# Performance work log

Measured on AMD Instinct MI355X. Metric: run time of the kernel, lower is better.

## Reference

```python
import jax, jax.numpy as jnp
import numpy as np

E = 16          # total experts (two halves of 8)
E_HALF = 8
K = 2           # top-k per token
CAP_FACTOR = 2  # expert capacity factor over the average load


def setup_inputs() -> dict:
    key = jax.random.key(0)
    ks = jax.random.split(key, 6)
    N, D, F = 16384, 1024, 1024  # tokens, d_model, d_ff (repo uses d_ff == d_model)
    s = 0.02
    return {
        "moe_inp": jax.random.normal(ks[0], (N, D), jnp.float32),
        "gate_w": jax.random.normal(ks[1], (D, E), jnp.float32) * s,   # gate Linear(d_model, 16)
        "gate_b": jnp.zeros((E,), jnp.float32),
        "route_w": jax.random.normal(ks[2], (D, 1), jnp.float32) * s,  # self.weights Linear(d_model, 1)
        "route_b": jnp.zeros((1,), jnp.float32),
        "W1": jax.random.normal(ks[3], (E, D, F), jnp.float32) * s,    # htoh4 per expert
        "b1": jnp.zeros((E, F), jnp.float32),
        "W2": jax.random.normal(ks[4], (E, F, D), jnp.float32) * s,    # h4toh per expert
        "b2": jnp.zeros((E, D), jnp.float32),
    }


def reference(moe_inp, gate_w, gate_b, route_w, route_b, W1, b1, W2, b2):
    N, D = moe_inp.shape
    # --- gate: logits over 16 experts; half 1 -> experts [0,8), half 2 -> experts [8,16)
    logits = moe_inp @ gate_w + gate_b                       # [N, E]
    val1, idx1 = jax.lax.top_k(logits[:, :E_HALF], K)        # [N, K]
    score1 = jax.nn.softmax(val1, axis=-1)
    val2, idx2 = jax.lax.top_k(logits[:, E_HALF:], K)
    score2 = jax.nn.softmax(val2, axis=-1)
    idx2 = idx2 + E_HALF                                     # shift into second expert range (gate_top_k_idx_2 + 8)
    # --- hard binary split of tokens via sigmoid(Linear(d,1)) > 0.5
    group1 = jax.nn.sigmoid(moe_inp @ route_w + route_b) > 0.5   # [N, 1]
    idx = jnp.where(group1, idx1, idx2)                      # [N, K] combined routing
    score = jnp.where(group1, score1, score2)                # [N, K]
    # --- dispatch: flatten (token, slot) pairs, capacity-bucket per expert
    T = N * K
    C = CAP_FACTOR * T // E                                  # expert capacity
    flat_idx = idx.reshape(-1)                               # [T]
    flat_x = jnp.repeat(moe_inp, K, axis=0)                  # [T, D]
    onehot = jax.nn.one_hot(flat_idx, E, dtype=jnp.int32)    # [T, E]
    pos_in_e = (jnp.cumsum(onehot, axis=0) * onehot).sum(axis=1) - 1  # [T] slot within expert
    valid = pos_in_e < C
    safe_pos = jnp.where(valid, pos_in_e, 0)
    buf = jnp.zeros((E, C, D), moe_inp.dtype).at[flat_idx, safe_pos].add(
        jnp.where(valid[:, None], flat_x, 0.0))              # [E, C, D] contiguous per-expert inputs
    # --- grouped expert FFN: relu(x W1 + b1) W2 + b2 (dropout = identity in eval)
    h = jax.nn.relu(jnp.einsum('ecd,edf->ecf', buf, W1) + b1[:, None, :])
    y = jnp.einsum('ecf,efd->ecd', h, W2) + b2[:, None, :]   # [E, C, D]
    # --- gather back and combine with gate scores
    y_flat = jnp.where(valid[:, None], y[flat_idx, safe_pos], 0.0)   # [T, D]
    out = (y_flat.reshape(N, K, D) * score[..., None]).sum(axis=1)   # [N, D]
    return out
```

## Files before the change

kernel.cpp:

```cpp
#include <hip/hip_runtime.h>
#include <hip/hip_bf16.h>
#include <stdint.h>

#define N_TOK 16384
#define DMODEL 1024
#define EXP 16
#define CAP 4096
#define TT 32768

typedef __bf16 bf16x8 __attribute__((ext_vector_type(8)));
typedef __bf16 bf16x4 __attribute__((ext_vector_type(4)));
typedef float  f32x4  __attribute__((ext_vector_type(4)));

__device__ __forceinline__ void gl_lds16(const void* g, void* s) {
  __builtin_amdgcn_global_load_lds(
      (__attribute__((address_space(1))) void*)(void*)g,
      (__attribute__((address_space(3))) void*)s, 16, 0, 0);
}

__device__ __forceinline__ float bfbits2f(unsigned short u) {
  return __uint_as_float(((unsigned)u) << 16);
}

#define FENCE asm volatile("" ::: "memory")
#define BAR() do { FENCE; __builtin_amdgcn_s_barrier(); FENCE; } while (0)

__global__ __launch_bounds__(256) void prep_kernel(const float* __restrict__ W1,
                                                   const float* __restrict__ W2,
                                                   __bf16* __restrict__ W1bt,
                                                   __bf16* __restrict__ W2bt,
                                                   const float* __restrict__ x,
                                                   const float* __restrict__ gw,
                                                   const float* __restrict__ gb,
                                                   const float* __restrict__ rw,
                                                   const float* __restrict__ rb,
                                                   int* __restrict__ idxo,
                                                   float* __restrict__ sco,
                                                   __bf16* __restrict__ Xb) {
  __shared__ float tile[64][65];
  int bid = blockIdx.x;
  int tid = threadIdx.x;
  if (bid % 9 != 8) {
    int cb = bid - (bid + 1) / 9;
    int tx = cb & 15;
    int ty = (cb >> 4) & 15;
    int e  = (cb >> 8) & 15;
    int which = (cb >> 12) & 1;
    const float* src = (which ? W2 : W1) + (size_t)e * DMODEL * DMODEL;
    __bf16*      dst = (which ? W2bt : W1bt) + (size_t)e * DMODEL * DMODEL;
    int r = tid >> 2;
    int cs = (tid & 3) * 16;
    int r0 = ty * 64, c0 = tx * 64;
    #pragma unroll
    for (int i = 0; i < 16; i += 4) {
      float4 v = *(const float4*)(src + (size_t)(r0 + r) * DMODEL + c0 + cs + i);
      tile[r][cs + i + 0] = v.x; tile[r][cs + i + 1] = v.y;
      tile[r][cs + i + 2] = v.z; tile[r][cs + i + 3] = v.w;
    }
    __syncthreads();
    bf16x8 o1, o2;
    #pragma unroll
    for (int i = 0; i < 8; i++) o1[i] = (__bf16)tile[cs + i][r];
    #pragma unroll
    for (int i = 0; i < 8; i++) o2[i] = (__bf16)tile[cs + 8 + i][r];
    {
      int n  = c0 + r;
      int g  = n >> 4, fr = n & 15;
      int k1 = r0 + cs;
      int c1 = k1 >> 5, fg1 = (k1 >> 3) & 3;
      int k2 = k1 + 8;
      int c2 = k2 >> 5, fg2 = (k2 >> 3) & 3;
      *(bf16x8*)(dst + ((size_t)(g * 32 + c1) * 512 + (fg1 * 16 + fr) * 8)) = o1;
      *(bf16x8*)(dst + ((size_t)(g * 32 + c2) * 512 + (fg2 * 16 + fr) * 8)) = o2;
    }
  } else {
    int g = bid / 9;
    int w = tid >> 6, lane = tid & 63;
    int n0t = g * 16 + w * 4;
    const float* xr0 = x + (size_t)(n0t + 0) * DMODEL;
    const float* xr1 = x + (size_t)(n0t + 1) * DMODEL;
    const float* xr2 = x + (size_t)(n0t + 2) * DMODEL;
    const float* xr3 = x + (size_t)(n0t + 3) * DMODEL;

    float acc0[17], acc1[17], acc2[17], acc3[17];
    #pragma unroll
    for (int j = 0; j < 17; j++) { acc0[j] = 0.f; acc1[j] = 0.f; acc2[j] = 0.f; acc3[j] = 0.f; }

    for (int c = 0; c < 4; c++) {
      int c0 = c * 256;
      #pragma unroll
      for (int dv = 0; dv < 4; dv++) {
        int d = c0 + dv * 64 + lane;
        float x0 = xr0[d], x1 = xr1[d], x2 = xr2[d], x3 = xr3[d];
        Xb[(size_t)(n0t + 0) * DMODEL + d] = (__bf16)x0;
        Xb[(size_t)(n0t + 1) * DMODEL + d] = (__bf16)x1;
        Xb[(size_t)(n0t + 2) * DMODEL + d] = (__bf16)x2;
        Xb[(size_t)(n0t + 3) * DMODEL + d] = (__bf16)x3;
        const float* gp = gw + (size_t)d * 16;
        float4 g0 = *(const float4*)(gp);
        float4 g1 = *(const float4*)(gp + 4);
        float4 g2 = *(const float4*)(gp + 8);
        float4 g3 = *(const float4*)(gp + 12);
        float rv = rw[d];
        float gj[16] = {g0.x, g0.y, g0.z, g0.w, g1.x, g1.y, g1.z, g1.w,
                        g2.x, g2.y, g2.z, g2.w, g3.x, g3.y, g3.z, g3.w};
        #pragma unroll
        for (int j = 0; j < 16; j++) {
          acc0[j] += x0 * gj[j]; acc1[j] += x1 * gj[j];
          acc2[j] += x2 * gj[j]; acc3[j] += x3 * gj[j];
        }
        acc0[16] += x0 * rv; acc1[16] += x1 * rv;
        acc2[16] += x2 * rv; acc3[16] += x3 * rv;
      }
    }

    #pragma unroll
    for (int o = 1; o < 64; o <<= 1) {
      #pragma unroll
      for (int j = 0; j < 17; j++) {
        acc0[j] += __shfl_xor(acc0[j], o);
        acc1[j] += __shfl_xor(acc1[j], o);
        acc2[j] += __shfl_xor(acc2[j], o);
        acc3[j] += __shfl_xor(acc3[j], o);
      }
    }
    if (lane == 0) {
      float* accs[4] = {acc0, acc1, acc2, acc3};
      #pragma unroll
      for (int tk = 0; tk < 4; tk++) {
        float* acc = accs[tk];
        int n = n0t + tk;
        float rv = acc[16] + rb[0];
        bool g1f = rv > 0.f;
        float c[8];
        #pragma unroll
        for (int j = 0; j < 8; j++)
          c[j] = (g1f ? acc[j] + gb[j] : acc[8 + j] + gb[8 + j]);
        int i1 = 0; float v1 = c[0];
        #pragma unroll
        for (int j = 1; j < 8; j++) { if (c[j] > v1) { v1 = c[j]; i1 = j; } }
        int i2 = -1; float v2 = -3.4e38f;
        #pragma unroll
        for (int j = 0; j < 8; j++) { if (j != i1 && c[j] > v2) { v2 = c[j]; i2 = j; } }
        float e2 = expf(v2 - v1);
        float den = 1.f + e2;
        int base = g1f ? 0 : 8;
        idxo[2 * n] = base + i1; idxo[2 * n + 1] = base + i2;
        sco[2 * n] = 1.f / den;  sco[2 * n + 1] = e2 / den;
      }
    }
  }
}

__global__ __launch_bounds__(1024) void scan_kernel(const int* __restrict__ idx,
                                                    float* __restrict__ sco,
                                                    int* __restrict__ rowlist,
                                                    int* __restrict__ cnt,
                                                    int* __restrict__ off) {
  __shared__ int hist[16 * 1024];
  int tid = threadIdx.x;
  #pragma unroll
  for (int e = 0; e < 16; e++) hist[e * 1024 + tid] = 0;
  __syncthreads();
  int base = tid * 32;
  for (int i = 0; i < 32; i++) {
    int e = idx[base + i];
    hist[e * 1024 + tid]++;
  }
  __syncthreads();
  int w = tid >> 6, lane = tid & 63;
  {
    int e = w;
    int running = 0;
    for (int cch = 0; cch < 16; cch++) {
      int v = hist[e * 1024 + cch * 64 + lane];
      int orig = v;
      #pragma unroll
      for (int o = 1; o < 64; o <<= 1) {
        int nv = __shfl_up(v, o);
        if (lane >= o) v += nv;
      }
      hist[e * 1024 + cch * 64 + lane] = running + v - orig;
      running += __shfl(v, 63);
    }
    if (lane == 0) cnt[e] = running;
  }
  __syncthreads();
  if (tid == 0) {
    int o = 0;
    for (int e = 0; e < 16; e++) {
      int c = cnt[e]; if (c > CAP) c = CAP;
      off[e] = o; cnt[e] = c; o += c;
    }
  }
  __syncthreads();
  for (int i = 0; i < 32; i++) {
    int t = base + i;
    int e = idx[t];
    int r = hist[e * 1024 + tid]++;
    if (r < CAP) rowlist[e * CAP + r] = t;
    else sco[t] = 0.f;
  }
}

#define GBM 128
#define GBN 128
#define GBK 32
#define NKT (DMODEL / GBK)

__global__ __launch_bounds__(256, 4) void moe_gemm(const __bf16* __restrict__ A,
                                                   const __bf16* __restrict__ Bf,
                                                   const float* __restrict__ bias,
                                                   __bf16* __restrict__ out,
                                                   const int* __restrict__ rowlist,
                                                   const int* __restrict__ cnt,
                                                   const int* __restrict__ off,
                                                   int mode) {
  __shared__ char lds[32768];
  int bx = blockIdx.x;
  int em = (bx & 7) * 64 + (bx >> 3);
  int e  = em >> 5;
  int m0 = (em & 31) * GBM;
  int ce = cnt[e];
  if (m0 >= ce) return;
  int n0 = blockIdx.y * GBN;
  int oe = off[e];
  int tid = threadIdx.x;

  const __bf16* aP[2];
  #pragma unroll
  for (int j = 0; j < 2; j++) {
    int lin = j * 256 + tid;
    int line = lin >> 3;
    int c = (lin & 7) ^ (line & 7);
    int srow = line * 2 + (c >> 2);
    int chunk = c & 3;
    int rr = m0 + srow; if (rr > ce - 1) rr = ce - 1;
    size_t arow;
    if (mode == 0) arow = (size_t)(rowlist[e * CAP + rr] >> 1);
    else           arow = (size_t)(oe + rr);
    aP[j] = A + arow * DMODEL + chunk * 8;
  }
  const __bf16* bP[2];
  int g0 = n0 >> 4;
  #pragma unroll
  for (int j = 0; j < 2; j++) {
    int lin = j * 256 + tid;
    int grp = lin >> 6;
    int ln  = lin & 63;
    bP[j] = Bf + (size_t)e * DMODEL * DMODEL
               + (size_t)((g0 + grp) * 32) * 512 + (size_t)ln * 8;
  }

  int w = tid >> 6, lane = tid & 63;
  int wr = (w >> 1) * 64;
  int wc = (w & 1) * 64;
  int fr = lane & 15, fg = lane >> 4;

  int gkA = ((((fr & 1) * 4) | fg) ^ ((fr >> 1) & 7)) * 16;
  int aRd = wr * 64 + (fr >> 1) * 128 + gkA;
  int bRd = 16384 + (w & 1) * 4096 + lane * 16;

  f32x4 acc[4][4];
  #pragma unroll
  for (int mi = 0; mi < 4; mi++)
    #pragma unroll
    for (int ni = 0; ni < 4; ni++)
      #pragma unroll
      for (int l = 0; l < 4; l++) acc[mi][ni][l] = 0.f;

  auto stA = [&](int s) {
    char* dst = lds + (s & 1) * 8192;
    gl_lds16(aP[0] + s * 32, dst + (size_t)tid * 16);
    gl_lds16(aP[1] + s * 32, dst + (size_t)(256 + tid) * 16);
  };
  auto stB = [&](int s) {
    char* dst = lds + 16384 + (s & 1) * 8192;
    gl_lds16(bP[0] + s * 512, dst + (size_t)tid * 16);
    gl_lds16(bP[1] + s * 512, dst + (size_t)(256 + tid) * 16);
  };

  stA(0); stB(0); stA(1); stB(1);
  asm volatile("s_waitcnt vmcnt(4)" ::: "memory");
  BAR();

  for (int t = 0; t < NKT; ++t) {
    const char* Ab = lds + (t & 1) * 8192 + aRd;
    const char* Bb = lds + (t & 1) * 8192 + bRd;

    bf16x8 af[4], bq[4];
    #pragma unroll
    for (int mi = 0; mi < 4; mi++) af[mi] = *(const bf16x8*)(Ab + mi * 1024);
    #pragma unroll
    for (int ni = 0; ni < 4; ni++) bq[ni] = *(const bf16x8*)(Bb + ni * 1024);
    asm volatile("s_waitcnt lgkmcnt(0)" ::: "memory");
    __builtin_amdgcn_sched_barrier(0);
    __builtin_amdgcn_s_setprio(1);
    #pragma unroll
    for (int mi = 0; mi < 4; mi++) {
      acc[mi][0] = __builtin_amdgcn_mfma_f32_16x16x32_bf16(af[mi], bq[0], acc[mi][0], 0, 0, 0);
      acc[mi][1] = __builtin_amdgcn_mfma_f32_16x16x32_bf16(af[mi], bq[1], acc[mi][1], 0, 0, 0);
    }
    __builtin_amdgcn_s_setprio(0);
    BAR();

    if (t <= NKT - 3) { stA(t + 2); stB(t + 2); }
    __builtin_amdgcn_s_setprio(1);
    #pragma unroll
    for (int mi = 0; mi < 4; mi++) {
      acc[mi][2] = __builtin_amdgcn_mfma_f32_16x16x32_bf16(af[mi], bq[2], acc[mi][2], 0, 0, 0);
      acc[mi][3] = __builtin_amdgcn_mfma_f32_16x16x32_bf16(af[mi], bq[3], acc[mi][3], 0, 0, 0);
    }
    __builtin_amdgcn_s_setprio(0);
    if (t <= NKT - 3)      asm volatile("s_waitcnt vmcnt(4)" ::: "memory");
    else if (t == NKT - 2) asm volatile("s_waitcnt vmcnt(0)" ::: "memory");
    BAR();
  }

  float bcol[4];
  #pragma unroll
  for (int ni = 0; ni < 4; ni++)
    bcol[ni] = bias[(size_t)e * DMODEL + n0 + wc + ni * 16 + fr];
  #pragma unroll
  for (int mi = 0; mi < 4; mi++) {
    #pragma unroll
    for (int r = 0; r < 4; r++) {
      int grow = m0 + wr + mi * 16 + fg * 4 + r;
      if (grow >= ce) continue;
      size_t orow = (mode == 0) ? (size_t)(oe + grow)
                                : (size_t)rowlist[e * CAP + grow];
      __bf16* op = out + orow * DMODEL + n0 + wc + fr;
      #pragma unroll
      for (int ni = 0; ni < 4; ni++) {
        float v = acc[mi][ni][r] + bcol[ni];
        if (mode == 0) v = fmaxf(v, 0.f);
        op[ni * 16] = (__bf16)v;
      }
    }
  }
}

__global__ __launch_bounds__(256) void combine_kernel(const __bf16* __restrict__ y,
                                                      const float* __restrict__ sco,
                                                      float* __restrict__ out) {
  int n = blockIdx.x;
  int d = threadIdx.x * 4;
  float s0 = sco[2 * n], s1 = sco[2 * n + 1];
  ushort4 a = *(const ushort4*)((const unsigned short*)(y + (size_t)(2 * n) * DMODEL + d));
  ushort4 b = *(const ushort4*)((const unsigned short*)(y + (size_t)(2 * n + 1) * DMODEL + d));
  float4 o;
  o.x = s0 * bfbits2f(a.x) + s1 * bfbits2f(b.x);
  o.y = s0 * bfbits2f(a.y) + s1 * bfbits2f(b.y);
  o.z = s0 * bfbits2f(a.z) + s1 * bfbits2f(b.z);
  o.w = s0 * bfbits2f(a.w) + s1 * bfbits2f(b.w);
  *(float4*)(out + (size_t)n * DMODEL + d) = o;
}

extern "C" void kernel_launch(void* const* d_in, const int* in_sizes, int n_in,
                              void* d_out, int out_size, void* d_ws, size_t ws_size,
                              hipStream_t stream) {
  const float* moe = (const float*)d_in[0];
  const float* gw  = (const float*)d_in[1];
  const float* gb  = (const float*)d_in[2];
  const float* rw  = (const float*)d_in[3];
  const float* rb  = (const float*)d_in[4];
  const float* W1  = (const float*)d_in[5];
  const float* b1  = (const float*)d_in[6];
  const float* W2  = (const float*)d_in[7];
  const float* b2  = (const float*)d_in[8];
  float* out = (float*)d_out;

  char* p = (char*)d_ws;
  __bf16* Xb   = (__bf16*)p; p += (size_t)N_TOK * DMODEL * 2;
  __bf16* W1bt = (__bf16*)p; p += (size_t)EXP * DMODEL * DMODEL * 2;
  __bf16* W2bt = (__bf16*)p; p += (size_t)EXP * DMODEL * DMODEL * 2;
  __bf16* hbuf = (__bf16*)p; p += (size_t)TT * DMODEL * 2;
  __bf16* ybuf = (__bf16*)p; p += (size_t)TT * DMODEL * 2;
  int*   idxb   = (int*)p;   p += (size_t)TT * 4;
  float* scoreb = (float*)p; p += (size_t)TT * 4;
  int*   rowlist = (int*)p;  p += (size_t)EXP * CAP * 4;
  int*   cntb    = (int*)p;  p += 64;
  int*   offb    = (int*)p;  p += 64;

  prep_kernel<<<dim3(9216), dim3(256), 0, stream>>>(W1, W2, W1bt, W2bt,
                                                    moe, gw, gb, rw, rb,
                                                    idxb, scoreb, Xb);
  scan_kernel<<<dim3(1), dim3(1024), 0, stream>>>(idxb, scoreb, rowlist, cntb, offb);
  moe_gemm<<<dim3(512, 8), dim3(256), 0, stream>>>(Xb, W1bt, b1, hbuf, rowlist, cntb, offb, 0);
  moe_gemm<<<dim3(512, 8), dim3(256), 0, stream>>>(hbuf, W2bt, b2, ybuf, rowlist, cntb, offb, 1);
  combine_kernel<<<dim3(16384), dim3(256), 0, stream>>>(ybuf, scoreb, out);
}
```

Measured before the change: 348.2 us.

## Replace single-block scan with atomic slot assignment in gating kernel

Removes the single-workgroup histogram/scan kernel and instead assigns each (token, slot) pair an expert capacity position via global atomicAdd directly in the gating part of the prep kernel. Expert offsets are recomputed in each GEMM block from clamped counts, and a tiny kernel zeroes the counters. This removes a serial, low-occupancy kernel from the critical path. In exchange, slot order within an expert becomes nondeterministic, so which tokens are dropped under overflow no longer follows token order, and row gathers lose sorted locality.

```diff
diff --git a/kernel.cpp b/kernel.cpp
--- a/kernel.cpp
+++ b/kernel.cpp
@@ -24,6 +24,10 @@
 
 #define FENCE asm volatile("" ::: "memory")
 #define BAR() do { FENCE; __builtin_amdgcn_s_barrier(); FENCE; } while (0)
+
+__global__ void zero16_kernel(int* __restrict__ cnt) {
+  if (threadIdx.x < EXP) cnt[threadIdx.x] = 0;
+}
 
 __global__ __launch_bounds__(256) void prep_kernel(const float* __restrict__ W1,
                                                    const float* __restrict__ W2,
@@ -34,7 +38,8 @@
                                                    const float* __restrict__ gb,
                                                    const float* __restrict__ rw,
                                                    const float* __restrict__ rb,
-                                                   int* __restrict__ idxo,
+                                                   int* __restrict__ cnt,
+                                                   int* __restrict__ rowlist,
                                                    float* __restrict__ sco,
                                                    __bf16* __restrict__ Xb) {
   __shared__ float tile[64][65];
@@ -145,61 +150,17 @@
         float e2 = expf(v2 - v1);
         float den = 1.f + e2;
         int base = g1f ? 0 : 8;
-        idxo[2 * n] = base + i1; idxo[2 * n + 1] = base + i2;
-        sco[2 * n] = 1.f / den;  sco[2 * n + 1] = e2 / den;
+        float s0v = 1.f / den, s1v = e2 / den;
+        sco[2 * n] = s0v;  sco[2 * n + 1] = s1v;
+        int e0 = base + i1, e1 = base + i2;
+        int r0 = atomicAdd(&cnt[e0], 1);
+        if (r0 < CAP) rowlist[e0 * CAP + r0] = 2 * n;
+        else sco[2 * n] = 0.f;
+        int r1 = atomicAdd(&cnt[e1], 1);
+        if (r1 < CAP) rowlist[e1 * CAP + r1] = 2 * n + 1;
+        else sco[2 * n + 1] = 0.f;
       }
     }
-  }
-}
-
-__global__ __launch_bounds__(1024) void scan_kernel(const int* __restrict__ idx,
-                                                    float* __restrict__ sco,
-                                                    int* __restrict__ rowlist,
-                                                    int* __restrict__ cnt,
-                                                    int* __restrict__ off) {
-  __shared__ int hist[16 * 1024];
-  int tid = threadIdx.x;
-  #pragma unroll
-  for (int e = 0; e < 16; e++) hist[e * 1024 + tid] = 0;
-  __syncthreads();
-  int base = tid * 32;
-  for (int i = 0; i < 32; i++) {
-    int e = idx[base + i];
-    hist[e * 1024 + tid]++;
-  }
-  __syncthreads();
-  int w = tid >> 6, lane = tid & 63;
-  {
-    int e = w;
-    int running = 0;
-    for (int cch = 0; cch < 16; cch++) {
-      int v = hist[e * 1024 + cch * 64 + lane];
-      int orig = v;
-      #pragma unroll
-      for (int o = 1; o < 64; o <<= 1) {
-        int nv = __shfl_up(v, o);
-        if (lane >= o) v += nv;
-      }
-      hist[e * 1024 + cch * 64 + lane] = running + v - orig;
-      running += __shfl(v, 63);
-    }
-    if (lane == 0) cnt[e] = running;
-  }
-  __syncthreads();
-  if (tid == 0) {
-    int o = 0;
-    for (int e = 0; e < 16; e++) {
-      int c = cnt[e]; if (c > CAP) c = CAP;
-      off[e] = o; cnt[e] = c; o += c;
-    }
-  }
-  __syncthreads();
-  for (int i = 0; i < 32; i++) {
-    int t = base + i;
-    int e = idx[t];
-    int r = hist[e * 1024 + tid]++;
-    if (r < CAP) rowlist[e * CAP + r] = t;
-    else sco[t] = 0.f;
   }
 }
 
@@ -214,17 +175,21 @@
                                                    __bf16* __restrict__ out,
                                                    const int* __restrict__ rowlist,
                                                    const int* __restrict__ cnt,
-                                                   const int* __restrict__ off,
                                                    int mode) {
   __shared__ char lds[32768];
   int bx = blockIdx.x;
   int em = (bx & 7) * 64 + (bx >> 3);
   int e  = em >> 5;
   int m0 = (em & 31) * GBM;
-  int ce = cnt[e];
+  int ce = 0, oe = 0;
+  #pragma unroll
+  for (int i = 0; i < EXP; i++) {
+    int ci = cnt[i]; if (ci > CAP) ci = CAP;
+    if (i < e) oe += ci;
+    if (i == e) ce = ci;
+  }
   if (m0 >= ce) return;
   int n0 = blockIdx.y * GBN;
-  int oe = off[e];
   int tid = threadIdx.x;
 
   const __bf16* aP[2];
@@ -376,17 +341,15 @@
   __bf16* W2bt = (__bf16*)p; p += (size_t)EXP * DMODEL * DMODEL * 2;
   __bf16* hbuf = (__bf16*)p; p += (size_t)TT * DMODEL * 2;
   __bf16* ybuf = (__bf16*)p; p += (size_t)TT * DMODEL * 2;
-  int*   idxb   = (int*)p;   p += (size_t)TT * 4;
   float* scoreb = (float*)p; p += (size_t)TT * 4;
   int*   rowlist = (int*)p;  p += (size_t)EXP * CAP * 4;
   int*   cntb    = (int*)p;  p += 64;
-  int*   offb    = (int*)p;  p += 64;
-
+
+  zero16_kernel<<<dim3(1), dim3(64), 0, stream>>>(cntb);
   prep_kernel<<<dim3(9216), dim3(256), 0, stream>>>(W1, W2, W1bt, W2bt,
                                                     moe, gw, gb, rw, rb,
-                                                    idxb, scoreb, Xb);
-  scan_kernel<<<dim3(1), dim3(1024), 0, stream>>>(idxb, scoreb, rowlist, cntb, offb);
-  moe_gemm<<<dim3(512, 8), dim3(256), 0, stream>>>(Xb, W1bt, b1, hbuf, rowlist, cntb, offb, 0);
-  moe_gemm<<<dim3(512, 8), dim3(256), 0, stream>>>(hbuf, W2bt, b2, ybuf, rowlist, cntb, offb, 1);
+                                                    cntb, rowlist, scoreb, Xb);
+  moe_gemm<<<dim3(512, 8), dim3(256), 0, stream>>>(Xb, W1bt, b1, hbuf, rowlist, cntb, 0);
+  moe_gemm<<<dim3(512, 8), dim3(256), 0, stream>>>(hbuf, W2bt, b2, ybuf, rowlist, cntb, 1);
   combine_kernel<<<dim3(16384), dim3(256), 0, stream>>>(ybuf, scoreb, out);
 }
```

Result: slower. 624.0 us (+79.2%).
